# Optimization experiments

Measured on AMD Instinct MI355X. Metric: run time of the kernel, lower is better.

Reference implementation:

```python
import jax, jax.numpy as jnp
import numpy as np


def setup_inputs() -> dict:
    key = jax.random.key(0)
    x = jax.random.normal(key, (2048, 32768), dtype=jnp.float32)
    return {"x": x, "k": 3}


def reference(x, k):
    # threshold = (k+1)-th largest value per row (sorted_values[:, k] in the original).
    # lax.top_k is the efficient partial-selection form of the full descending sort.
    topk_vals, _ = jax.lax.top_k(x, k + 1)          # [B, k+1]
    threshold = topk_vals[:, k:k + 1]               # [B, 1], broadcasts over last dim
    mask = x >= threshold                           # [B, N] bool
    return jnp.where(mask, x * 10, x)
```

## Files before the change

### kernel.cpp

```cpp
#include <hip/hip_runtime.h>
#include <math.h>

constexpr int NCOLS = 32768;
constexpr int BLOCK = 256;
constexpr int TOPN  = 8;

__device__ inline void merge8(float* a, const float* b) {
    float s[TOPN];
#pragma unroll
    for (int i = 0; i < TOPN; i++) s[i] = fmaxf(a[i], b[TOPN - 1 - i]);
#pragma unroll
    for (int i = 0; i < 4; i++) {
        float hi = fmaxf(s[i], s[i + 4]);
        float lo = fminf(s[i], s[i + 4]);
        s[i] = hi; s[i + 4] = lo;
    }
#pragma unroll
    for (int g = 0; g < 8; g += 4)
#pragma unroll
        for (int i = 0; i < 2; i++) {
            float hi = fmaxf(s[g + i], s[g + i + 2]);
            float lo = fminf(s[g + i], s[g + i + 2]);
            s[g + i] = hi; s[g + i + 2] = lo;
        }
#pragma unroll
    for (int g = 0; g < 8; g += 2) {
        float hi = fmaxf(s[g], s[g + 1]);
        float lo = fminf(s[g], s[g + 1]);
        s[g] = hi; s[g + 1] = lo;
    }
#pragma unroll
    for (int i = 0; i < TOPN; i++) a[i] = s[i];
}

__device__ inline void insert8(float* v, float x) {
    if (x > v[7]) {
        v[7] = x;
#pragma unroll
        for (int i = 7; i > 0; i--) {
            float hi = fmaxf(v[i - 1], v[i]);
            float lo = fminf(v[i - 1], v[i]);
            v[i - 1] = hi; v[i] = lo;
        }
    }
}

__global__ __launch_bounds__(BLOCK) void topk_scale_kernel(
    const float* __restrict__ x, const int* __restrict__ kptr,
    float* __restrict__ out) {
    __shared__ float lds[BLOCK][TOPN + 1];

    const int row = blockIdx.x;
    const int tid = threadIdx.x;
    const float4* __restrict__ xrow =
        reinterpret_cast<const float4*>(x + (size_t)row * NCOLS);
    float4* __restrict__ orow =
        reinterpret_cast<float4*>(out + (size_t)row * NCOLS);
    const int nvec = NCOLS / 4;

    float v[TOPN];
#pragma unroll
    for (int i = 0; i < TOPN; i++) v[i] = -INFINITY;

    for (int i = tid; i < nvec; i += BLOCK) {
        float4 p = xrow[i];
        insert8(v, p.x);
        insert8(v, p.y);
        insert8(v, p.z);
        insert8(v, p.w);
    }

#pragma unroll
    for (int i = 0; i < TOPN; i++) lds[tid][i] = v[i];
    __syncthreads();

    for (int stride = BLOCK / 2; stride > 0; stride >>= 1) {
        if (tid < stride) {
            float a[TOPN], b[TOPN];
#pragma unroll
            for (int i = 0; i < TOPN; i++) {
                a[i] = lds[tid][i];
                b[i] = lds[tid + stride][i];
            }
            merge8(a, b);
#pragma unroll
            for (int i = 0; i < TOPN; i++) lds[tid][i] = a[i];
        }
        __syncthreads();
    }

    int k = *kptr;
    if (k > TOPN - 1) k = TOPN - 1;
    const float thr = lds[0][k];

    for (int i = tid; i < nvec; i += BLOCK) {
        float4 p = xrow[i];
        float4 o;
        o.x = (p.x >= thr) ? p.x * 10.0f : p.x;
        o.y = (p.y >= thr) ? p.y * 10.0f : p.y;
        o.z = (p.z >= thr) ? p.z * 10.0f : p.z;
        o.w = (p.w >= thr) ? p.w * 10.0f : p.w;
        orow[i] = o;
    }
}

extern "C" void kernel_launch(void* const* d_in, const int* in_sizes, int n_in,
                              void* d_out, int out_size, void* d_ws, size_t ws_size,
                              hipStream_t stream) {
    const float* x = (const float*)d_in[0];
    const int* k = (const int*)d_in[1];
    float* out = (float*)d_out;
    const int nrows = in_sizes[0] / NCOLS;
    topk_scale_kernel<<<nrows, BLOCK, 0, stream>>>(x, k, out);
}
```

Measured before the change: 483.3 us.

## Replace per-element insertion with sorting-network batching and wave-shuffle reduction

The per-element branchy insert into a top-8 list is replaced by sorting four float4 loads with small sorting networks, then merging the sorted lists into the running top-8 branch-free. The LDS tree reduction across 256 threads, with its many barriers, becomes an xor-shuffle butterfly within each wave plus a small cross-wave merge done redundantly by every thread. The loops are fully unrolled so several loads are in flight at once, and the output uses nontemporal stores. Register pressure goes up, and the branch-free merges do a fixed amount of work per element even though few elements would ever pass the old insert test.

```diff
diff --git a/kernel.cpp b/kernel.cpp
--- a/kernel.cpp
+++ b/kernel.cpp
@@ -4,103 +4,126 @@
 constexpr int NCOLS = 32768;
 constexpr int BLOCK = 256;
 constexpr int TOPN  = 8;
+constexpr int NV    = NCOLS / 4 / BLOCK;
+constexpr int PC1   = 4;
+constexpr int NC1   = NV / PC1;
+constexpr int PC2   = 8;
+constexpr int NC2   = NV / PC2;
+constexpr int NWAVE = BLOCK / 64;
 
-__device__ inline void merge8(float* a, const float* b) {
+typedef float vf4 __attribute__((ext_vector_type(4)));
+
+__device__ __forceinline__ void ce(float& a, float& b) {
+    float hi = fmaxf(a, b), lo = fminf(a, b);
+    a = hi; b = lo;
+}
+
+__device__ __forceinline__ void merge8(float* a, const float* b) {
     float s[TOPN];
 #pragma unroll
     for (int i = 0; i < TOPN; i++) s[i] = fmaxf(a[i], b[TOPN - 1 - i]);
 #pragma unroll
-    for (int i = 0; i < 4; i++) {
-        float hi = fmaxf(s[i], s[i + 4]);
-        float lo = fminf(s[i], s[i + 4]);
-        s[i] = hi; s[i + 4] = lo;
-    }
-#pragma unroll
-    for (int g = 0; g < 8; g += 4)
-#pragma unroll
-        for (int i = 0; i < 2; i++) {
-            float hi = fmaxf(s[g + i], s[g + i + 2]);
-            float lo = fminf(s[g + i], s[g + i + 2]);
-            s[g + i] = hi; s[g + i + 2] = lo;
-        }
-#pragma unroll
-    for (int g = 0; g < 8; g += 2) {
-        float hi = fmaxf(s[g], s[g + 1]);
-        float lo = fminf(s[g], s[g + 1]);
-        s[g] = hi; s[g + 1] = lo;
-    }
+    for (int i = 0; i < 4; i++) ce(s[i], s[i + 4]);
+    ce(s[0], s[2]); ce(s[1], s[3]); ce(s[4], s[6]); ce(s[5], s[7]);
+    ce(s[0], s[1]); ce(s[2], s[3]); ce(s[4], s[5]); ce(s[6], s[7]);
 #pragma unroll
     for (int i = 0; i < TOPN; i++) a[i] = s[i];
 }
 
-__device__ inline void insert8(float* v, float x) {
-    if (x > v[7]) {
-        v[7] = x;
-#pragma unroll
-        for (int i = 7; i > 0; i--) {
-            float hi = fmaxf(v[i - 1], v[i]);
-            float lo = fminf(v[i - 1], v[i]);
-            v[i - 1] = hi; v[i] = lo;
-        }
-    }
+__device__ __forceinline__ void sort4(const float4 p, float* d) {
+    float hi01 = fmaxf(p.x, p.y), lo01 = fminf(p.x, p.y);
+    float hi23 = fmaxf(p.z, p.w), lo23 = fminf(p.z, p.w);
+    d[0] = fmaxf(hi01, hi23);
+    float t2 = fminf(hi01, hi23);
+    float t1 = fmaxf(lo01, lo23);
+    d[3] = fminf(lo01, lo23);
+    d[1] = fmaxf(t1, t2);
+    d[2] = fminf(t1, t2);
+}
+
+__device__ __forceinline__ void merge44(const float* a, const float* b, float* s) {
+    s[0] = a[0]; s[1] = a[1]; s[2] = a[2]; s[3] = a[3];
+    s[4] = b[3]; s[5] = b[2]; s[6] = b[1]; s[7] = b[0];
+    ce(s[0], s[4]); ce(s[1], s[5]); ce(s[2], s[6]); ce(s[3], s[7]);
+    ce(s[0], s[2]); ce(s[1], s[3]); ce(s[4], s[6]); ce(s[5], s[7]);
+    ce(s[0], s[1]); ce(s[2], s[3]); ce(s[4], s[5]); ce(s[6], s[7]);
 }
 
 __global__ __launch_bounds__(BLOCK) void topk_scale_kernel(
     const float* __restrict__ x, const int* __restrict__ kptr,
     float* __restrict__ out) {
-    __shared__ float lds[BLOCK][TOPN + 1];
+    __shared__ float wtop[NWAVE][TOPN];
 
     const int row = blockIdx.x;
     const int tid = threadIdx.x;
     const float4* __restrict__ xrow =
         reinterpret_cast<const float4*>(x + (size_t)row * NCOLS);
-    float4* __restrict__ orow =
-        reinterpret_cast<float4*>(out + (size_t)row * NCOLS);
-    const int nvec = NCOLS / 4;
+    vf4* __restrict__ orow =
+        reinterpret_cast<vf4*>(out + (size_t)row * NCOLS);
+
+    int k = *kptr;
+    if (k > TOPN - 1) k = TOPN - 1;
 
     float v[TOPN];
 #pragma unroll
     for (int i = 0; i < TOPN; i++) v[i] = -INFINITY;
 
-    for (int i = tid; i < nvec; i += BLOCK) {
-        float4 p = xrow[i];
-        insert8(v, p.x);
-        insert8(v, p.y);
-        insert8(v, p.z);
-        insert8(v, p.w);
+#pragma unroll
+    for (int c = 0; c < NC1; c++) {
+        float4 b[PC1];
+#pragma unroll
+        for (int j = 0; j < PC1; j++) b[j] = xrow[tid + (c * PC1 + j) * BLOCK];
+
+        float s0[4], s1[4], s2[4], s3[4];
+        sort4(b[0], s0); sort4(b[1], s1); sort4(b[2], s2); sort4(b[3], s3);
+        float m0[TOPN], m1[TOPN];
+        merge44(s0, s1, m0);
+        merge44(s2, s3, m1);
+        merge8(m0, m1);
+        merge8(v, m0);
     }
 
 #pragma unroll
-    for (int i = 0; i < TOPN; i++) lds[tid][i] = v[i];
+    for (int msk = 1; msk < 64; msk <<= 1) {
+        float b[TOPN];
+#pragma unroll
+        for (int i = 0; i < TOPN; i++) b[i] = __shfl_xor(v[i], msk, 64);
+        merge8(v, b);
+    }
+
+    const int wid = tid >> 6;
+    if ((tid & 63) == 0) {
+#pragma unroll
+        for (int i = 0; i < TOPN; i++) wtop[wid][i] = v[i];
+    }
     __syncthreads();
 
-    for (int stride = BLOCK / 2; stride > 0; stride >>= 1) {
-        if (tid < stride) {
-            float a[TOPN], b[TOPN];
+    float a[TOPN];
 #pragma unroll
-            for (int i = 0; i < TOPN; i++) {
-                a[i] = lds[tid][i];
-                b[i] = lds[tid + stride][i];
-            }
-            merge8(a, b);
+    for (int i = 0; i < TOPN; i++) a[i] = wtop[0][i];
 #pragma unroll
-            for (int i = 0; i < TOPN; i++) lds[tid][i] = a[i];
+    for (int w = 1; w < NWAVE; w++) {
+        float bb[TOPN];
+#pragma unroll
+        for (int i = 0; i < TOPN; i++) bb[i] = wtop[w][i];
+        merge8(a, bb);
+    }
+    const float thr = a[k];
+
+#pragma unroll
+    for (int c = 0; c < NC2; c++) {
+        float4 p[PC2];
+#pragma unroll
+        for (int j = 0; j < PC2; j++) p[j] = xrow[tid + (c * PC2 + j) * BLOCK];
+#pragma unroll
+        for (int j = 0; j < PC2; j++) {
+            vf4 o;
+            o.x = (p[j].x >= thr) ? p[j].x * 10.0f : p[j].x;
+            o.y = (p[j].y >= thr) ? p[j].y * 10.0f : p[j].y;
+            o.z = (p[j].z >= thr) ? p[j].z * 10.0f : p[j].z;
+            o.w = (p[j].w >= thr) ? p[j].w * 10.0f : p[j].w;
+            __builtin_nontemporal_store(o, &orow[tid + (c * PC2 + j) * BLOCK]);
         }
-        __syncthreads();
-    }
-
-    int k = *kptr;
-    if (k > TOPN - 1) k = TOPN - 1;
-    const float thr = lds[0][k];
-
-    for (int i = tid; i < nvec; i += BLOCK) {
-        float4 p = xrow[i];
-        float4 o;
-        o.x = (p.x >= thr) ? p.x * 10.0f : p.x;
-        o.y = (p.y >= thr) ? p.y * 10.0f : p.y;
-        o.z = (p.z >= thr) ? p.z * 10.0f : p.z;
-        o.w = (p.w >= thr) ? p.w * 10.0f : p.w;
-        orow[i] = o;
     }
 }
 
```

After: 460.6 us. 4.7% less time.
